# Performance work log

Hardware: AMD Instinct MI355X
Metric: run time of the kernel (lower is better)

The kernel has to match this reference:

```python
import jax, jax.numpy as jnp
import numpy as np
import math

B, L, D = 2, 2048, 2048
H, DH = 16, 128
R = 16
WIN = 512
EPS = 1e-6


def setup_inputs() -> dict:
    key = jax.random.key(0)
    ks = jax.random.split(key, 16)
    def rn(k, shape, s=1.0):
        return jax.random.normal(k, shape, dtype=jnp.float32) * s
    d_in_std = 1.0 / math.sqrt(D)
    return {
        "x": rn(ks[0], (B, L, D)),
        "norm_w": jnp.ones((D,), jnp.float32),
        "wq": rn(ks[1], (H * DH, D), d_in_std),
        "wk": rn(ks[2], (H * DH, D), d_in_std),
        "wv": rn(ks[3], (H * DH, D), d_in_std),
        "wo": rn(ks[4], (D, H * DH), d_in_std),
        "qA": rn(ks[5], (R, D), 0.02), "qB": rn(ks[6], (H * DH, R), 0.02),
        "kA": rn(ks[7], (R, D), 0.02), "kB": rn(ks[8], (H * DH, R), 0.02),
        "vA": rn(ks[9], (R, D), 0.02), "vB": rn(ks[10], (H * DH, R), 0.02),
        "oA": rn(ks[11], (R, H * DH), 0.02), "oB": rn(ks[12], (D, R), 0.02),
    }


def _lora_proj(h, Wb, A, Bm, scale):
    # y = h @ Wb^T + ((h @ A^T) @ Bm^T) * scale
    return h @ Wb.T + (h @ A.T) @ Bm.T * scale


def _rope_freqs(seq_len, d_head):
    half = d_head // 2
    theta = 1.0 / (10000.0 ** (jnp.arange(half, dtype=jnp.float32) / half))
    freqs = jnp.arange(seq_len, dtype=jnp.float32)[:, None] * theta[None, :]  # (L, half)
    emb = jnp.concatenate([freqs, freqs], axis=-1)  # (L, d_head)
    return jnp.cos(emb), jnp.sin(emb)


def _apply_rope(x, cos, sin):
    # x: (B, H, L, d_head); cos/sin: (L, d_head)
    half = x.shape[-1] // 2
    x1, x2 = x[..., :half], x[..., half:]
    rotated = jnp.concatenate([-x2, x1], axis=-1)
    return x * cos[None, None] + rotated * sin[None, None]


def reference(x, norm_w, wq, wk, wv, wo, qA, qB, kA, kB, vA, vB, oA, oB):
    lora_scale = 1.0 / qA.shape[0]
    residual = x
    # RMSNorm
    h = x * jax.lax.rsqrt(jnp.mean(x * x, axis=-1, keepdims=True) + EPS) * norm_w
    # LoRA-fused projections
    Q = _lora_proj(h, wq, qA, qB, lora_scale)
    K = _lora_proj(h, wk, kA, kB, lora_scale)
    V = _lora_proj(h, wv, vA, vB, lora_scale)
    b, l, _ = x.shape
    Q = Q.reshape(b, l, H, DH).transpose(0, 2, 1, 3)
    K = K.reshape(b, l, H, DH).transpose(0, 2, 1, 3)
    V = V.reshape(b, l, H, DH).transpose(0, 2, 1, 3)
    cos, sin = _rope_freqs(l, DH)
    Q = _apply_rope(Q, cos, sin)
    K = _apply_rope(K, cos, sin)
    # sliding-window causal additive mask (L, L)
    i = jnp.arange(l)[:, None]
    j = jnp.arange(l)[None, :]
    valid = (j <= i) & (j >= i - WIN + 1)
    mask = jnp.where(valid, 0.0, -jnp.inf).astype(x.dtype)
    scores = jnp.einsum("bhqd,bhkd->bhqk", Q, K) / math.sqrt(DH)
    attn = jax.nn.softmax(scores + mask[None, None], axis=-1)
    out = jnp.einsum("bhqk,bhkd->bhqd", attn, V)
    out = out.transpose(0, 2, 1, 3).reshape(b, l, H * DH)
    out = _lora_proj(out, wo, oA, oB, lora_scale)
    return residual + out
```

## Files before the change

### kernel.cpp

```cpp
#include <hip/hip_runtime.h>
#include <hip/hip_bf16.h>

#define LNUM 2048
#define DNUM 2048
#define HNUM 16
#define DHNUM 128
#define MTOK 4096
#define WINSZ 512

typedef __attribute__((ext_vector_type(8))) short bf16x8;
typedef __attribute__((ext_vector_type(4))) short bf16x4;
typedef __attribute__((ext_vector_type(4))) float f32x4;

#define GLOBAL_AS __attribute__((address_space(1)))
#define LDS_AS __attribute__((address_space(3)))
#define BARX asm volatile("s_barrier" ::: "memory")

__device__ __forceinline__ unsigned short f2bf(float f) {
  union { float f; unsigned u; } v; v.f = f;
  unsigned r = v.u + 0x7FFFu + ((v.u >> 16) & 1u);
  return (unsigned short)(r >> 16);
}
__device__ __forceinline__ float bf2f(unsigned short h) {
  union { unsigned u; float f; } v; v.u = ((unsigned)h) << 16;
  return v.f;
}

__global__ __launch_bounds__(256) void weff_k(
    const float* __restrict__ w0, const float* __restrict__ w1,
    const float* __restrict__ w2, const float* __restrict__ w3,
    const float* __restrict__ b0, const float* __restrict__ b1,
    const float* __restrict__ b2, const float* __restrict__ b3,
    const float* __restrict__ a0, const float* __restrict__ a1,
    const float* __restrict__ a2, const float* __restrict__ a3,
    unsigned short* __restrict__ o0, unsigned short* __restrict__ o1,
    unsigned short* __restrict__ o2, unsigned short* __restrict__ o3,
    float s) {
  const int z = blockIdx.z;
  const float* W = z==0?w0:z==1?w1:z==2?w2:w3;
  const float* Bm = z==0?b0:z==1?b1:z==2?b2:b3;
  const float* Am = z==0?a0:z==1?a1:z==2?a2:a3;
  unsigned short* out = z==0?o0:z==1?o1:z==2?o2:o3;

  const int col = blockIdx.x * 1024 + threadIdx.x * 4;
  const int row0 = blockIdx.y * 64;

  float4 av[16];
  #pragma unroll
  for (int j = 0; j < 16; j++) av[j] = *(const float4*)(Am + (size_t)j * DNUM + col);

  for (int r = 0; r < 64; r++) {
    const int n = row0 + r;
    const float* brow = Bm + (size_t)n * 16;
    float dx = 0.f, dy = 0.f, dz = 0.f, dw = 0.f;
    #pragma unroll
    for (int j = 0; j < 16; j++) {
      const float bj = brow[j];
      dx = fmaf(bj, av[j].x, dx); dy = fmaf(bj, av[j].y, dy);
      dz = fmaf(bj, av[j].z, dz); dw = fmaf(bj, av[j].w, dw);
    }
    const float4 wv = *(const float4*)(W + (size_t)n * DNUM + col);
    ushort4 o;
    o.x = f2bf(wv.x + s*dx); o.y = f2bf(wv.y + s*dy);
    o.z = f2bf(wv.z + s*dz); o.w = f2bf(wv.w + s*dw);
    *(ushort4*)(out + (size_t)n * DNUM + col) = o;
  }
}

__global__ __launch_bounds__(256) void rmsnorm_k(const float* __restrict__ x,
                                                 const float* __restrict__ w,
                                                 unsigned short* __restrict__ h) {
  const int row = blockIdx.x;
  const int t = threadIdx.x;
  const float4* xr = (const float4*)(x + (size_t)row * DNUM);
  float4 v0 = xr[t];
  float4 v1 = xr[t + 256];
  float ss = v0.x*v0.x + v0.y*v0.y + v0.z*v0.z + v0.w*v0.w +
             v1.x*v1.x + v1.y*v1.y + v1.z*v1.z + v1.w*v1.w;
  #pragma unroll
  for (int off = 32; off > 0; off >>= 1) ss += __shfl_xor(ss, off);
  __shared__ float red[4];
  if ((t & 63) == 0) red[t >> 6] = ss;
  __syncthreads();
  const float r = rsqrtf((red[0]+red[1]+red[2]+red[3]) * (1.0f/DNUM) + 1e-6f);
  const float4* wr4 = (const float4*)w;
  float4 w0 = wr4[t], w1 = wr4[t+256];
  ushort4 o0, o1;
  o0.x = f2bf(v0.x*r*w0.x); o0.y = f2bf(v0.y*r*w0.y);
  o0.z = f2bf(v0.z*r*w0.z); o0.w = f2bf(v0.w*r*w0.w);
  o1.x = f2bf(v1.x*r*w1.x); o1.y = f2bf(v1.y*r*w1.y);
  o1.z = f2bf(v1.z*r*w1.z); o1.w = f2bf(v1.w*r*w1.w);
  ushort4* hp = (ushort4*)(h + (size_t)row * DNUM);
  hp[t] = o0; hp[t + 256] = o1;
}

__global__ __launch_bounds__(512, 1) void gemmqkv_k(
    const unsigned short* __restrict__ Am,
    const unsigned short* __restrict__ Wall,
    unsigned short* __restrict__ Oall)
{
  const int row0 = blockIdx.y * 256;
  const int col0 = blockIdx.x * 192;
  const int tid = threadIdx.x;
  const int wv = tid >> 6, lane = tid & 63;
  const int wr = wv >> 2, wc = wv & 3;
  const int g = lane >> 4, r4 = lane & 15;

  __shared__ unsigned short lds[57344];

  const int rp = lane >> 2;
  const int sg8 = ((lane & 3) ^ ((rp >> 1) & 3)) * 8;

  auto stage = [&](int buf, int k0) {
    #pragma unroll
    for (int q = 0; q < 4; q++) {
      const int c = q*8 + wv;
      const int kh = c & 1, rc = c >> 1;
      const unsigned short* ga = Am + (size_t)(row0 + rc*16 + rp) * DNUM + k0 + kh*32 + sg8;
      __builtin_amdgcn_global_load_lds((const GLOBAL_AS void*)ga,
          (LDS_AS void*)&lds[buf*16384 + (kh*16 + rc)*512], 16, 0, 0);
    }
    #pragma unroll
    for (int q = 0; q < 3; q++) {
      const int c = q*8 + wv;
      const int kh = c & 1, rc = c >> 1;
      const unsigned short* gb = Wall + (size_t)(col0 + rc*16 + rp) * DNUM + k0 + kh*32 + sg8;
      __builtin_amdgcn_global_load_lds((const GLOBAL_AS void*)gb,
          (LDS_AS void*)&lds[32768 + buf*12288 + (kh*12 + rc)*512], 16, 0, 0);
    }
  };

  f32x4 acc[8][3];
  #pragma unroll
  for (int m = 0; m < 8; m++)
    #pragma unroll
    for (int n = 0; n < 3; n++) acc[m][n] = f32x4{0.f,0.f,0.f,0.f};

  const int cg = (g ^ ((r4 >> 1) & 3)) * 8;

  auto compute = [&](int buf) {
    #pragma unroll
    for (int kh = 0; kh < 2; kh++) {
      const unsigned short* As = &lds[buf*16384 + kh*8192];
      const unsigned short* Bs = &lds[32768 + buf*12288 + kh*6144];
      bf16x8 af[8], bb[3];
      #pragma unroll
      for (int m = 0; m < 8; m++)
        af[m] = *(const bf16x8*)&As[(wr*8 + m)*512 + r4*32 + cg];
      #pragma unroll
      for (int n = 0; n < 3; n++)
        bb[n] = *(const bf16x8*)&Bs[(wc*3 + n)*512 + r4*32 + cg];
      #pragma unroll
      for (int m = 0; m < 8; m++)
        #pragma unroll
        for (int n = 0; n < 3; n++)
          acc[m][n] = __builtin_amdgcn_mfma_f32_16x16x32_bf16(af[m], bb[n], acc[m][n], 0, 0, 0);
    }
  };

  stage(0, 0);
  const int nt = DNUM / 64;
  for (int t = 0; t < nt; t++) {
    if (t < nt - 1) {
      stage((t + 1) & 1, (t + 1) * 64);
      asm volatile("s_waitcnt vmcnt(7)" ::: "memory");
    } else {
      asm volatile("s_waitcnt vmcnt(0)" ::: "memory");
    }
    BARX;
    compute(t & 1);
    BARX;
  }

  #pragma unroll
  for (int m = 0; m < 8; m++) {
    #pragma unroll
    for (int rg = 0; rg < 4; rg++) {
      const int row = row0 + wr*128 + m*16 + 4*g + rg;
      #pragma unroll
      for (int n = 0; n < 3; n++) {
        const int colg = col0 + wc*48 + n*16 + r4;
        const int z = colg >> 11, c = colg & 2047;
        Oall[((size_t)z * MTOK + row) * DNUM + c] = f2bf(acc[m][n][rg]);
      }
    }
  }
}

__global__ __launch_bounds__(256, 3) void gemm_k(
    const unsigned short* __restrict__ Am,
    const unsigned short* __restrict__ W0,
    const float* __restrict__ resid, float* __restrict__ Of)
{
  const unsigned short* W = W0;

  const int row0 = blockIdx.y * 128;
  const int col0 = blockIdx.x * 128;
  const int tid = threadIdx.x;
  const int wv = tid >> 6, lane = tid & 63;
  const int wr = wv >> 1, wc = wv & 1;
  const int g = lane >> 4, r4 = lane & 15;

  __shared__ unsigned short lds[2][2][4096];

  f32x4 acc[4][4];
  #pragma unroll
  for (int m=0;m<4;m++)
    #pragma unroll
    for (int n=0;n<4;n++) acc[m][n] = f32x4{0.f,0.f,0.f,0.f};

  auto stage = [&](int buf, int k0) {
    #pragma unroll
    for (int qq = 0; qq < 2; qq++) {
      const int chunk = wv*2 + qq;
      const int rp = chunk*16 + (lane >> 2);
      const int cl = (lane & 3) ^ ((rp >> 1) & 3);
      const unsigned short* ga = Am + (size_t)(row0 + rp) * DNUM + k0 + cl*8;
      __builtin_amdgcn_global_load_lds((const GLOBAL_AS void*)ga,
          (LDS_AS void*)&lds[buf][0][chunk*512], 16, 0, 0);
      const unsigned short* gb = W + (size_t)(col0 + rp) * DNUM + k0 + cl*8;
      __builtin_amdgcn_global_load_lds((const GLOBAL_AS void*)gb,
          (LDS_AS void*)&lds[buf][1][chunk*512], 16, 0, 0);
    }
  };

  stage(0, 0);
  const int nk = DNUM / 32;
  for (int kt = 0; kt < nk; kt++) {
    __syncthreads();
    if (kt + 1 < nk) stage((kt+1) & 1, (kt+1)*32);
    const unsigned short* As = &lds[kt&1][0][0];
    const unsigned short* Bs = &lds[kt&1][1][0];
    bf16x8 af[4], bb[4];
    #pragma unroll
    for (int m = 0; m < 4; m++) {
      const int R = wr*64 + m*16 + r4;
      af[m] = *(const bf16x8*)((const char*)As + R*64 + ((g ^ ((R>>1)&3))*16));
    }
    #pragma unroll
    for (int n = 0; n < 4; n++) {
      const int R = wc*64 + n*16 + r4;
      bb[n] = *(const bf16x8*)((const char*)Bs + R*64 + ((g ^ ((R>>1)&3))*16));
    }
    #pragma unroll
    for (int m = 0; m < 4; m++)
      #pragma unroll
      for (int n = 0; n < 4; n++)
        acc[m][n] = __builtin_amdgcn_mfma_f32_16x16x32_bf16(af[m], bb[n], acc[m][n], 0, 0, 0);
  }

  #pragma unroll
  for (int m = 0; m < 4; m++) {
    #pragma unroll
    for (int rg = 0; rg < 4; rg++) {
      const int row = row0 + wr*64 + m*16 + 4*g + rg;
      #pragma unroll
      for (int n = 0; n < 4; n++) {
        const int col = col0 + wc*64 + n*16 + r4;
        Of[(size_t)row * DNUM + col] = acc[m][n][rg] + resid[(size_t)row * DNUM + col];
      }
    }
  }
}

__global__ __launch_bounds__(256) void rope_k(unsigned short* __restrict__ Qm,
                                              unsigned short* __restrict__ Km) {
  const int u = blockIdx.x * 256 + threadIdx.x;
  const int t2 = u & 31;
  const int hh = (u >> 5) & (HNUM-1);
  const int i = u >> 9;
  const int l = i & (LNUM - 1);
  const int d0 = 2 * t2;
  const float C = 0.14391156831212787f;
  const float th0 = __expf(-(float)d0 * C);
  const float th1 = __expf(-(float)(d0+1) * C);
  float sn0, cs0, sn1, cs1;
  __sincosf((float)l * th0, &sn0, &cs0);
  __sincosf((float)l * th1, &sn1, &cs1);
  const size_t base = (size_t)i * DNUM + hh * DHNUM + d0;
  const float qs = 0.08838834764831845f;

  unsigned qa = *(const unsigned*)(Qm + base);
  unsigned qb = *(const unsigned*)(Qm + base + 64);
  float a0 = bf2f((unsigned short)qa), a1 = bf2f((unsigned short)(qa >> 16));
  float b0 = bf2f((unsigned short)qb), b1 = bf2f((unsigned short)(qb >> 16));
  unsigned lo = (unsigned)f2bf((a0*cs0 - b0*sn0) * qs) | ((unsigned)f2bf((a1*cs1 - b1*sn1) * qs) << 16);
  unsigned hi = (unsigned)f2bf((b0*cs0 + a0*sn0) * qs) | ((unsigned)f2bf((b1*cs1 + a1*sn1) * qs) << 16);
  *(unsigned*)(Qm + base) = lo;
  *(unsigned*)(Qm + base + 64) = hi;

  unsigned ka = *(const unsigned*)(Km + base);
  unsigned kb = *(const unsigned*)(Km + base + 64);
  a0 = bf2f((unsigned short)ka); a1 = bf2f((unsigned short)(ka >> 16));
  b0 = bf2f((unsigned short)kb); b1 = bf2f((unsigned short)(kb >> 16));
  lo = (unsigned)f2bf(a0*cs0 - b0*sn0) | ((unsigned)f2bf(a1*cs1 - b1*sn1) << 16);
  hi = (unsigned)f2bf(b0*cs0 + a0*sn0) | ((unsigned)f2bf(b1*cs1 + a1*sn1) << 16);
  *(unsigned*)(Km + base) = lo;
  *(unsigned*)(Km + base + 64) = hi;
}

__global__ __launch_bounds__(256) void attn_k(const unsigned short* __restrict__ Q,
                                              const unsigned short* __restrict__ K,
                                              const unsigned short* __restrict__ V,
                                              unsigned short* __restrict__ O) {
  __shared__ unsigned short Kls[8192];
  __shared__ unsigned short Vt[8704];
  const int tid = threadIdx.x, wv = tid >> 6, lane = tid & 63;
  const int g = lane >> 4, r4 = lane & 15;
  const int bidx = blockIdx.x;
  const int q4 = bidx & 31, hh = (bidx >> 5) & 15, b = bidx >> 9;
  const int q_base = q4 * 64;
  const int q0 = q_base + wv * 16;
  const size_t bh = (size_t)b * LNUM * DNUM + (size_t)hh * DHNUM;

  bf16x8 qf[4];
  {
    const unsigned short* qr = Q + bh + (size_t)(q0 + r4) * DNUM;
    #pragma unroll
    for (int dc = 0; dc < 4; dc++) qf[dc] = *(const bf16x8*)(qr + dc*32 + g*8);
  }
  f32x4 oacc[8];
  #pragma unroll
  for (int c = 0; c < 8; c++) oacc[c] = f32x4{0.f,0.f,0.f,0.f};
  float mrun = -1e30f, lrun = 0.f;

  const int qi = q0 + r4;
  const int lo_key = (q_base >= WINSZ) ? (q_base - WINSZ + 1) : 0;
  const int t_lo = lo_key >> 6, t_hi = q_base >> 6;

  const int rp = lane >> 2;
  const int sg = (((lane & 3) ^ ((rp >> 1) & 3))) * 8;
  const int cgr = (g ^ ((r4 >> 1) & 3)) * 8;

  const int vc = wv*8 + (lane >> 3);
  const int vd = lane & 7;

  for (int t64 = t_lo; t64 <= t_hi; t64++) {
    const int k64 = t64 * 64;
    __syncthreads();
    #pragma unroll
    for (int q = 0; q < 4; q++) {
      const unsigned short* src = K + bh + (size_t)(k64 + wv*16 + rp) * DNUM + q*32 + sg;
      __builtin_amdgcn_global_load_lds((const GLOBAL_AS void*)src,
          (LDS_AS void*)&Kls[(q*4 + wv)*512], 16, 0, 0);
    }
    #pragma unroll
    for (int p = 0; p < 2; p++) {
      const int d0 = (vd + 8*p) * 8;
      const unsigned short* vp = V + bh + (size_t)(k64 + 2*vc) * DNUM + d0;
      uint4 va = *(const uint4*)vp;
      uint4 vb = *(const uint4*)(vp + DNUM);
      const unsigned short* as = (const unsigned short*)&va;
      const unsigned short* bs = (const unsigned short*)&vb;
      #pragma unroll
      for (int j = 0; j < 8; j++) {
        *(unsigned*)&Vt[(d0 + j)*68 + 2*vc] = (unsigned)as[j] | ((unsigned)bs[j] << 16);
      }
    }
    __syncthreads();

    #pragma unroll
    for (int kts = 0; kts < 4; kts++) {
      const int k0s = k64 + kts*16;
      if (k0s > q0 + 15 || k0s + 15 < q0 - (WINSZ - 1)) continue;
      f32x4 st = f32x4{0.f,0.f,0.f,0.f};
      #pragma unroll
      for (int dc = 0; dc < 4; dc++) {
        const bf16x8 kf = *(const bf16x8*)&Kls[(dc*4 + kts)*512 + r4*32 + cgr];
        st = __builtin_amdgcn_mfma_f32_16x16x32_bf16(kf, qf[dc], st, 0, 0, 0);
      }
      const int kj = k0s + 4*g;
      const float sv0 = (kj   <= qi && kj   > qi - WINSZ) ? st[0] : -1e30f;
      const float sv1 = (kj+1 <= qi && kj+1 > qi - WINSZ) ? st[1] : -1e30f;
      const float sv2 = (kj+2 <= qi && kj+2 > qi - WINSZ) ? st[2] : -1e30f;
      const float sv3 = (kj+3 <= qi && kj+3 > qi - WINSZ) ? st[3] : -1e30f;
      float pmax = fmaxf(fmaxf(sv0, sv1), fmaxf(sv2, sv3));
      pmax = fmaxf(pmax, __shfl_xor(pmax, 16));
      pmax = fmaxf(pmax, __shfl_xor(pmax, 32));
      const float mnew = fmaxf(mrun, pmax);
      const float sc_old = __expf(mrun - mnew);
      const float p0 = __expf(sv0 - mnew), p1 = __expf(sv1 - mnew);
      const float p2 = __expf(sv2 - mnew), p3 = __expf(sv3 - mnew);
      float psum = p0 + p1 + p2 + p3;
      psum += __shfl_xor(psum, 16);
      psum += __shfl_xor(psum, 32);
      lrun = lrun * sc_old + psum;
      mrun = mnew;
      bf16x4 pf;
      pf[0] = (short)f2bf(p0); pf[1] = (short)f2bf(p1);
      pf[2] = (short)f2bf(p2); pf[3] = (short)f2bf(p3);
      #pragma unroll
      for (int c = 0; c < 8; c++) {
        oacc[c][0] *= sc_old; oacc[c][1] *= sc_old;
        oacc[c][2] *= sc_old; oacc[c][3] *= sc_old;
      }
      #pragma unroll
      for (int dblk = 0; dblk < 8; dblk++) {
        const bf16x4 vf = *(const bf16x4*)&Vt[(dblk*16 + r4)*68 + kts*16 + 4*g];
        oacc[dblk] = __builtin_amdgcn_mfma_f32_16x16x16bf16_1k(vf, pf, oacc[dblk], 0, 0, 0);
      }
    }
  }

  __syncthreads();
  unsigned short* scr = &Vt[wv * 2176];
  const float inv = 1.0f / lrun;
  #pragma unroll
  for (int dblk = 0; dblk < 8; dblk++) {
    #pragma unroll
    for (int rg = 0; rg < 4; rg++) {
      scr[r4*136 + dblk*16 + 4*g + rg] = f2bf(oacc[dblk][rg] * inv);
    }
  }
  #pragma unroll
  for (int p = 0; p < 4; p++) {
    const int qq = p*4 + g;
    const uint4 vvv = *(const uint4*)(scr + qq*136 + r4*8);
    *(uint4*)(O + bh + (size_t)(q0 + qq) * DNUM + r4*8) = vvv;
  }
}

extern "C" void kernel_launch(void* const* d_in, const int* in_sizes, int n_in,
                              void* d_out, int out_size, void* d_ws, size_t ws_size,
                              hipStream_t stream) {
  (void)in_sizes; (void)n_in; (void)out_size; (void)ws_size;
  const float* x     = (const float*)d_in[0];
  const float* normw = (const float*)d_in[1];
  const float* wq = (const float*)d_in[2];
  const float* wk = (const float*)d_in[3];
  const float* wvm = (const float*)d_in[4];
  const float* wo = (const float*)d_in[5];
  const float* qA = (const float*)d_in[6];
  const float* qB = (const float*)d_in[7];
  const float* kA = (const float*)d_in[8];
  const float* kB = (const float*)d_in[9];
  const float* vA = (const float*)d_in[10];
  const float* vB = (const float*)d_in[11];
  const float* oA = (const float*)d_in[12];
  const float* oB = (const float*)d_in[13];

  char* w = (char*)d_ws;
  const size_t SZ = (size_t)MTOK * DNUM * 2;
  unsigned short* h  = (unsigned short*)(w);
  unsigned short* Qb = (unsigned short*)(w + SZ);
  unsigned short* Kb = (unsigned short*)(w + 2*SZ);
  unsigned short* Vb = (unsigned short*)(w + 3*SZ);
  unsigned short* AO = (unsigned short*)(w + 4*SZ);
  unsigned short* Wq = (unsigned short*)(w + 5*SZ);
  unsigned short* Wk = Wq + (size_t)DNUM*DNUM;
  unsigned short* Wv = Wk + (size_t)DNUM*DNUM;
  unsigned short* Wo = Wv + (size_t)DNUM*DNUM;

  const float lscale = 1.0f / 16.0f;

  weff_k<<<dim3(2, 32, 4), 256, 0, stream>>>(wq, wk, wvm, wo,
                                             qB, kB, vB, oB,
                                             qA, kA, vA, oA,
                                             Wq, Wk, Wv, Wo, lscale);
  rmsnorm_k<<<dim3(4096), 256, 0, stream>>>(x, normw, h);
  gemmqkv_k<<<dim3(32, 16), 512, 0, stream>>>(h, Wq, Qb);
  rope_k<<<dim3(8192), 256, 0, stream>>>(Qb, Kb);
  attn_k<<<dim3(1024), 256, 0, stream>>>(Qb, Kb, Vb, AO);
  gemm_k<<<dim3(16,32,1), 256, 0, stream>>>(AO, Wo, x, (float*)d_out);
}
```

Measured before the change: 268.3 us.

## Restructure output projection GEMM to 256x128 tiles with 64-wide K stages

Replaces the 128x128, 256-thread output-projection GEMM with a 512-thread kernel that computes 256x128 tiles and stages 64 elements of K per iteration. A partial vmcnt wait lets the next stage's loads overlap the current compute, and the per-step syncthreads is replaced with explicit barriers. The aim is more reuse per LDS load and fewer loop iterations and barriers. In exchange it uses 96KB of LDS and allows one block per CU, and the grid shrinks to 256 blocks, which may leave CUs underfilled.

```diff
diff --git a/kernel.cpp b/kernel.cpp
--- a/kernel.cpp
+++ b/kernel.cpp
@@ -187,76 +187,92 @@
   }
 }
 
-__global__ __launch_bounds__(256, 3) void gemm_k(
+__global__ __launch_bounds__(512, 1) void gemmo_k(
     const unsigned short* __restrict__ Am,
-    const unsigned short* __restrict__ W0,
+    const unsigned short* __restrict__ W,
     const float* __restrict__ resid, float* __restrict__ Of)
 {
-  const unsigned short* W = W0;
-
-  const int row0 = blockIdx.y * 128;
+  const int row0 = blockIdx.y * 256;
   const int col0 = blockIdx.x * 128;
   const int tid = threadIdx.x;
   const int wv = tid >> 6, lane = tid & 63;
-  const int wr = wv >> 1, wc = wv & 1;
+  const int wr = wv >> 2, wc = wv & 3;
   const int g = lane >> 4, r4 = lane & 15;
 
-  __shared__ unsigned short lds[2][2][4096];
-
-  f32x4 acc[4][4];
-  #pragma unroll
-  for (int m=0;m<4;m++)
-    #pragma unroll
-    for (int n=0;n<4;n++) acc[m][n] = f32x4{0.f,0.f,0.f,0.f};
+  __shared__ unsigned short lds[49152];
+
+  const int rp = lane >> 2;
+  const int sg8 = ((lane & 3) ^ ((rp >> 1) & 3)) * 8;
 
   auto stage = [&](int buf, int k0) {
     #pragma unroll
-    for (int qq = 0; qq < 2; qq++) {
-      const int chunk = wv*2 + qq;
-      const int rp = chunk*16 + (lane >> 2);
-      const int cl = (lane & 3) ^ ((rp >> 1) & 3);
-      const unsigned short* ga = Am + (size_t)(row0 + rp) * DNUM + k0 + cl*8;
+    for (int q = 0; q < 4; q++) {
+      const int c = q*8 + wv;
+      const int kh = c & 1, rc = c >> 1;
+      const unsigned short* ga = Am + (size_t)(row0 + rc*16 + rp) * DNUM + k0 + kh*32 + sg8;
       __builtin_amdgcn_global_load_lds((const GLOBAL_AS void*)ga,
-          (LDS_AS void*)&lds[buf][0][chunk*512], 16, 0, 0);
-      const unsigned short* gb = W + (size_t)(col0 + rp) * DNUM + k0 + cl*8;
+          (LDS_AS void*)&lds[buf*16384 + (kh*16 + rc)*512], 16, 0, 0);
+    }
+    #pragma unroll
+    for (int q = 0; q < 2; q++) {
+      const int c = q*8 + wv;
+      const int kh = c & 1, rc = c >> 1;
+      const unsigned short* gb = W + (size_t)(col0 + rc*16 + rp) * DNUM + k0 + kh*32 + sg8;
       __builtin_amdgcn_global_load_lds((const GLOBAL_AS void*)gb,
-          (LDS_AS void*)&lds[buf][1][chunk*512], 16, 0, 0);
+          (LDS_AS void*)&lds[32768 + buf*8192 + (kh*8 + rc)*512], 16, 0, 0);
     }
   };
 
+  f32x4 acc[8][2];
+  #pragma unroll
+  for (int m = 0; m < 8; m++)
+    #pragma unroll
+    for (int n = 0; n < 2; n++) acc[m][n] = f32x4{0.f,0.f,0.f,0.f};
+
+  const int cg = (g ^ ((r4 >> 1) & 3)) * 8;
+
+  auto compute = [&](int buf) {
+    #pragma unroll
+    for (int kh = 0; kh < 2; kh++) {
+      const unsigned short* As = &lds[buf*16384 + kh*8192];
+      const unsigned short* Bs = &lds[32768 + buf*8192 + kh*4096];
+      bf16x8 af[8], bb[2];
+      #pragma unroll
+      for (int m = 0; m < 8; m++)
+        af[m] = *(const bf16x8*)&As[(wr*8 + m)*512 + r4*32 + cg];
+      #pragma unroll
+      for (int n = 0; n < 2; n++)
+        bb[n] = *(const bf16x8*)&Bs[(wc*2 + n)*512 + r4*32 + cg];
+      #pragma unroll
+      for (int m = 0; m < 8; m++)
+        #pragma unroll
+        for (int n = 0; n < 2; n++)
+          acc[m][n] = __builtin_amdgcn_mfma_f32_16x16x32_bf16(af[m], bb[n], acc[m][n], 0, 0, 0);
+    }
+  };
+
   stage(0, 0);
-  const int nk = DNUM / 32;
-  for (int kt = 0; kt < nk; kt++) {
-    __syncthreads();
-    if (kt + 1 < nk) stage((kt+1) & 1, (kt+1)*32);
-    const unsigned short* As = &lds[kt&1][0][0];
-    const unsigned short* Bs = &lds[kt&1][1][0];
-    bf16x8 af[4], bb[4];
-    #pragma unroll
-    for (int m = 0; m < 4; m++) {
-      const int R = wr*64 + m*16 + r4;
-      af[m] = *(const bf16x8*)((const char*)As + R*64 + ((g ^ ((R>>1)&3))*16));
-    }
-    #pragma unroll
-    for (int n = 0; n < 4; n++) {
-      const int R = wc*64 + n*16 + r4;
-      bb[n] = *(const bf16x8*)((const char*)Bs + R*64 + ((g ^ ((R>>1)&3))*16));
-    }
-    #pragma unroll
-    for (int m = 0; m < 4; m++)
-      #pragma unroll
-      for (int n = 0; n < 4; n++)
-        acc[m][n] = __builtin_amdgcn_mfma_f32_16x16x32_bf16(af[m], bb[n], acc[m][n], 0, 0, 0);
-  }
-
-  #pragma unroll
-  for (int m = 0; m < 4; m++) {
+  const int nt = DNUM / 64;
+  for (int t = 0; t < nt; t++) {
+    if (t < nt - 1) {
+      stage((t + 1) & 1, (t + 1) * 64);
+      asm volatile("s_waitcnt vmcnt(6)" ::: "memory");
+    } else {
+      asm volatile("s_waitcnt vmcnt(0)" ::: "memory");
+    }
+    BARX;
+    compute(t & 1);
+    BARX;
+  }
+
+  #pragma unroll
+  for (int m = 0; m < 8; m++) {
     #pragma unroll
     for (int rg = 0; rg < 4; rg++) {
-      const int row = row0 + wr*64 + m*16 + 4*g + rg;
-      #pragma unroll
-      for (int n = 0; n < 4; n++) {
-        const int col = col0 + wc*64 + n*16 + r4;
+      const int row = row0 + wr*128 + m*16 + 4*g + rg;
+      #pragma unroll
+      for (int n = 0; n < 2; n++) {
+        const int col = col0 + wc*32 + n*16 + r4;
         Of[(size_t)row * DNUM + col] = acc[m][n][rg] + resid[(size_t)row * DNUM + col];
       }
     }
@@ -461,5 +477,5 @@
   gemmqkv_k<<<dim3(32, 16), 512, 0, stream>>>(h, Wq, Qb);
   rope_k<<<dim3(8192), 256, 0, stream>>>(Qb, Kb);
   attn_k<<<dim3(1024), 256, 0, stream>>>(Qb, Kb, Vb, AO);
-  gemm_k<<<dim3(16,32,1), 256, 0, stream>>>(AO, Wo, x, (float*)d_out);
-}
+  gemmo_k<<<dim3(16, 16), 512, 0, stream>>>(AO, Wo, x, (float*)d_out);
+}
```

After: 260.2 us. 3.0% less time.
